# Kernel optimization log

Measured on AMD Instinct MI355X. Metric: run time of the kernel, lower is better.

## Reference

```python
import jax, jax.numpy as jnp
import numpy as np

B, T, C, H = 2, 2048, 1024, 16
D = C // H  # head dim = 64


def setup_inputs() -> dict:
    key = jax.random.key(0)
    ks = jax.random.split(key, 5)
    s = 0.02
    return {
        "x": jax.random.normal(ks[0], (B, T, C), dtype=jnp.float32),
        "c_attn_w": jax.random.normal(ks[1], (C, 3 * C), dtype=jnp.float32) * s,
        "c_attn_b": jax.random.normal(ks[2], (3 * C,), dtype=jnp.float32) * s,
        "c_proj_w": jax.random.normal(ks[3], (C, C), dtype=jnp.float32) * s,
        "c_proj_b": jax.random.normal(ks[4], (C,), dtype=jnp.float32) * s,
    }


def reference(x, c_attn_w, c_attn_b, c_proj_w, c_proj_b):
    b, t, c = x.shape
    # GPT-2 Conv1D: x @ W + b
    qkv = x @ c_attn_w + c_attn_b                      # [B,T,3C]
    q, k, v = jnp.split(qkv, 3, axis=-1)
    # [B,H,T,D]
    q = q.reshape(b, t, H, D).transpose(0, 2, 1, 3)
    k = k.reshape(b, t, H, D).transpose(0, 2, 1, 3)
    v = v.reshape(b, t, H, D).transpose(0, 2, 1, 3)
    scale = 1.0 / jnp.sqrt(jnp.float32(D))
    scores = jnp.einsum("bhqd,bhkd->bhqk", q, k) * scale  # [B,H,T,T]
    causal = jnp.tril(jnp.ones((t, t), dtype=bool))
    scores = jnp.where(causal, scores, jnp.float32(-jnp.inf))
    attn = jax.nn.softmax(scores, axis=-1)
    # drop_rate = 0.0 -> dropout is identity
    y = jnp.einsum("bhqk,bhkd->bhqd", attn, v)          # [B,H,T,D]
    y = y.transpose(0, 2, 1, 3).reshape(b, t, c)
    return y @ c_proj_w + c_proj_b
```

## Files before the change

kernel.cpp:

```cpp
#include <hip/hip_runtime.h>

#define B_ 2
#define T_ 2048
#define C_ 1024
#define H_ 16
#define D_ 64
#define M_ (B_ * T_)
#define NQKV_ (3 * C_)

typedef unsigned short us16;
typedef short bf16x8 __attribute__((ext_vector_type(8)));
typedef float f32x4 __attribute__((ext_vector_type(4)));

__device__ __forceinline__ f32x4 mfma16(bf16x8 a, bf16x8 b, f32x4 c) {
    return __builtin_amdgcn_mfma_f32_16x16x32_bf16(a, b, c, 0, 0, 0);
}

__device__ __forceinline__ us16 f2bf(float f) {
    union { float f; unsigned int u; } v; v.f = f;
    unsigned int r = v.u + 0x7fffu + ((v.u >> 16) & 1u);
    return (us16)(r >> 16);
}

__global__ __launch_bounds__(256) void cvt_bf16(
    const float* __restrict__ in, us16* __restrict__ out, int n8)
{
    const int i = blockIdx.x * blockDim.x + threadIdx.x;
    if (i >= n8) return;
    const float4 a = ((const float4*)in)[2 * i];
    const float4 b = ((const float4*)in)[2 * i + 1];
    ushort4 lo = { f2bf(a.x), f2bf(a.y), f2bf(a.z), f2bf(a.w) };
    ushort4 hi = { f2bf(b.x), f2bf(b.y), f2bf(b.z), f2bf(b.w) };
    ((ushort4*)out)[2 * i] = lo;
    ((ushort4*)out)[2 * i + 1] = hi;
}

__global__ __launch_bounds__(256) void transpose_cvt(
    const float* __restrict__ W, us16* __restrict__ Wt, int K, int N)
{
    __shared__ float tile[32][33];
    const int n0 = blockIdx.x * 32, k0 = blockIdx.y * 32;
    const int t = threadIdx.x;
    {
        const int k = t >> 3, n4 = (t & 7) * 4;
        const float4 v = *(const float4*)(W + (size_t)(k0 + k) * N + n0 + n4);
        tile[k][n4 + 0] = v.x; tile[k][n4 + 1] = v.y;
        tile[k][n4 + 2] = v.z; tile[k][n4 + 3] = v.w;
    }
    __syncthreads();
    {
        const int n = t >> 3, k4 = (t & 7) * 4;
        ushort4 o = { f2bf(tile[k4 + 0][n]), f2bf(tile[k4 + 1][n]),
                      f2bf(tile[k4 + 2][n]), f2bf(tile[k4 + 3][n]) };
        *(ushort4*)(Wt + (size_t)(n0 + n) * K + k0 + k4) = o;
    }
}

__global__ __launch_bounds__(256) void gemm_bf16(
    const us16* __restrict__ A, const us16* __restrict__ Bt,
    const float* __restrict__ bias, void* __restrict__ Cout,
    int M, int N, int K, int out_bf16)
{
    __shared__ __align__(16) us16 smem[2 * 128 * 72];
    us16* sA = smem;
    us16* sB = smem + 128 * 72;

    const int tid = threadIdx.x;
    const int lane = tid & 63, wave = tid >> 6;
    const int wr = wave >> 1, wc = wave & 1;
    const int cq = lane & 15, quad = lane >> 4;
    const int m0 = blockIdx.y * 128, n0 = blockIdx.x * 128;

    f32x4 acc[4][4];
    #pragma unroll
    for (int i = 0; i < 4; ++i)
        #pragma unroll
        for (int j = 0; j < 4; ++j)
            acc[i][j] = (f32x4){0.f, 0.f, 0.f, 0.f};

    for (int k0 = 0; k0 < K; k0 += 64) {
        #pragma unroll
        for (int p = 0; p < 4; ++p) {
            const int chunk = p * 256 + tid;
            const int r = chunk >> 3, c8 = (chunk & 7) * 8;
            const uint4 va = *(const uint4*)(A + (size_t)(m0 + r) * K + k0 + c8);
            *(uint4*)(sA + r * 72 + c8) = va;
            const uint4 vb = *(const uint4*)(Bt + (size_t)(n0 + r) * K + k0 + c8);
            *(uint4*)(sB + r * 72 + c8) = vb;
        }
        __syncthreads();

        #pragma unroll
        for (int kk = 0; kk < 64; kk += 32) {
            const int ko = kk + quad * 8;
            bf16x8 af[4], bfg[4];
            #pragma unroll
            for (int i = 0; i < 4; ++i) {
                af[i]  = *(const bf16x8*)(sA + (wr * 64 + i * 16 + cq) * 72 + ko);
                bfg[i] = *(const bf16x8*)(sB + (wc * 64 + i * 16 + cq) * 72 + ko);
            }
            #pragma unroll
            for (int mi = 0; mi < 4; ++mi)
                #pragma unroll
                for (int ni = 0; ni < 4; ++ni)
                    acc[mi][ni] = mfma16(af[mi], bfg[ni], acc[mi][ni]);
        }
        __syncthreads();
    }

    if (out_bf16) {
        us16* Cs = smem;
        #pragma unroll
        for (int mi = 0; mi < 4; ++mi)
            #pragma unroll
            for (int ni = 0; ni < 4; ++ni) {
                const int n = n0 + wc * 64 + ni * 16 + cq;
                const float bv = bias[n];
                #pragma unroll
                for (int r = 0; r < 4; ++r)
                    Cs[(wr * 64 + mi * 16 + quad * 4 + r) * 136 +
                       wc * 64 + ni * 16 + cq] = f2bf(acc[mi][ni][r] + bv);
            }
        __syncthreads();
        us16* Co = (us16*)Cout;
        #pragma unroll
        for (int p = 0; p < 8; ++p) {
            const int chunk = p * 256 + tid;
            const int r = chunk >> 4, c = (chunk & 15) * 8;
            *(uint4*)(Co + (size_t)(m0 + r) * N + n0 + c) =
                *(const uint4*)(Cs + r * 136 + c);
        }
    } else {
        float* Co = (float*)Cout;
        #pragma unroll
        for (int mi = 0; mi < 4; ++mi)
            #pragma unroll
            for (int ni = 0; ni < 4; ++ni) {
                const int n = n0 + wc * 64 + ni * 16 + cq;
                const float bv = bias[n];
                #pragma unroll
                for (int r = 0; r < 4; ++r)
                    Co[(size_t)(m0 + wr * 64 + mi * 16 + quad * 4 + r) * N + n] =
                        acc[mi][ni][r] + bv;
            }
    }
}

__global__ __launch_bounds__(256) void attn_mfma(
    const us16* __restrict__ qkv, us16* __restrict__ y)
{
    __shared__ __align__(16) us16 Ks[64][72];
    __shared__ __align__(16) us16 Vt[64][72];
    __shared__ __align__(16) us16 Ps[64][72];

    const int tid = threadIdx.x;
    const int lane = tid & 63, wave = tid >> 6;
    const int cq = lane & 15, quad = lane >> 4;
    const int bh = blockIdx.x;
    const int qt = (int)gridDim.y - 1 - (int)blockIdx.y;
    const int b = bh >> 4, h = bh & 15;

    const us16* base = qkv + (size_t)b * T_ * NQKV_ + h * D_;

    bf16x8 qf[2];
    {
        const us16* qrow = base + (size_t)(qt * 64 + wave * 16 + cq) * NQKV_;
        qf[0] = *(const bf16x8*)(qrow + quad * 8);
        qf[1] = *(const bf16x8*)(qrow + 32 + quad * 8);
    }

    f32x4 o[4];
    #pragma unroll
    for (int j = 0; j < 4; ++j) o[j] = (f32x4){0.f, 0.f, 0.f, 0.f};
    float m_run[4], l_run[4];
    #pragma unroll
    for (int r = 0; r < 4; ++r) { m_run[r] = -1e30f; l_run[r] = 0.f; }

    const int t2 = tid & 31, dc = tid >> 5;

    for (int kt = 0; kt <= qt; ++kt) {
        __syncthreads();
        #pragma unroll
        for (int p = 0; p < 2; ++p) {
            const int chunk = p * 256 + tid;
            const int r = chunk >> 3, c8 = (chunk & 7) * 8;
            const uint4 v = *(const uint4*)(base + (size_t)(kt * 64 + r) * NQKV_ + C_ + c8);
            *(uint4*)(&Ks[r][c8]) = v;
        }
        {
            const us16* vp = base + (size_t)(kt * 64 + 2 * t2) * NQKV_ + 2 * C_ + dc * 8;
            const uint4 u0 = *(const uint4*)vp;
            const uint4 u1 = *(const uint4*)(vp + NQKV_);
            const us16* p0 = (const us16*)&u0;
            const us16* p1 = (const us16*)&u1;
            #pragma unroll
            for (int j = 0; j < 8; ++j) {
                const unsigned int packed =
                    (unsigned int)p0[j] | ((unsigned int)p1[j] << 16);
                *(unsigned int*)(&Vt[dc * 8 + j][2 * t2]) = packed;
            }
        }
        __syncthreads();

        f32x4 s[4];
        #pragma unroll
        for (int j = 0; j < 4; ++j) {
            const bf16x8 kf0 = *(const bf16x8*)(&Ks[j * 16 + cq][quad * 8]);
            const bf16x8 kf1 = *(const bf16x8*)(&Ks[j * 16 + cq][32 + quad * 8]);
            f32x4 t = (f32x4){0.f, 0.f, 0.f, 0.f};
            t = mfma16(qf[0], kf0, t);
            t = mfma16(qf[1], kf1, t);
            s[j] = t;
        }

        #pragma unroll
        for (int j = 0; j < 4; ++j)
            #pragma unroll
            for (int r = 0; r < 4; ++r)
                s[j][r] *= 0.125f;
        if (kt == qt) {
            const int qloc = wave * 16 + quad * 4;
            #pragma unroll
            for (int j = 0; j < 4; ++j) {
                const int kloc = j * 16 + cq;
                #pragma unroll
                for (int r = 0; r < 4; ++r)
                    if (kloc > qloc + r) s[j][r] = -1e30f;
            }
        }

        #pragma unroll
        for (int r = 0; r < 4; ++r) {
            float mx = fmaxf(fmaxf(s[0][r], s[1][r]), fmaxf(s[2][r], s[3][r]));
            #pragma unroll
            for (int off = 8; off >= 1; off >>= 1)
                mx = fmaxf(mx, __shfl_xor(mx, off));
            const float m_new = fmaxf(m_run[r], mx);
            const float alpha = __expf(m_run[r] - m_new);
            float sum = 0.f;
            #pragma unroll
            for (int j = 0; j < 4; ++j) {
                s[j][r] = __expf(s[j][r] - m_new);
                sum += s[j][r];
            }
            #pragma unroll
            for (int off = 8; off >= 1; off >>= 1)
                sum += __shfl_xor(sum, off);
            l_run[r] = l_run[r] * alpha + sum;
            m_run[r] = m_new;
            #pragma unroll
            for (int j = 0; j < 4; ++j) o[j][r] *= alpha;
        }

        #pragma unroll
        for (int j = 0; j < 4; ++j)
            #pragma unroll
            for (int r = 0; r < 4; ++r)
                Ps[wave * 16 + quad * 4 + r][j * 16 + cq] = f2bf(s[j][r]);

        const bf16x8 pf0 = *(const bf16x8*)(&Ps[wave * 16 + cq][quad * 8]);
        const bf16x8 pf1 = *(const bf16x8*)(&Ps[wave * 16 + cq][32 + quad * 8]);
        #pragma unroll
        for (int dt = 0; dt < 4; ++dt) {
            const bf16x8 vf0 = *(const bf16x8*)(&Vt[dt * 16 + cq][quad * 8]);
            const bf16x8 vf1 = *(const bf16x8*)(&Vt[dt * 16 + cq][32 + quad * 8]);
            o[dt] = mfma16(pf0, vf0, o[dt]);
            o[dt] = mfma16(pf1, vf1, o[dt]);
        }
    }

    #pragma unroll
    for (int r = 0; r < 4; ++r) {
        const float inv = 1.0f / l_run[r];
        const int row = qt * 64 + wave * 16 + quad * 4 + r;
        #pragma unroll
        for (int dt = 0; dt < 4; ++dt)
            y[(size_t)(b * T_ + row) * C_ + h * D_ + dt * 16 + cq] =
                f2bf(o[dt][r] * inv);
    }
}

extern "C" void kernel_launch(void* const* d_in, const int* in_sizes, int n_in,
                              void* d_out, int out_size, void* d_ws, size_t ws_size,
                              hipStream_t stream)
{
    const float* x  = (const float*)d_in[0];
    const float* aw = (const float*)d_in[1];
    const float* ab = (const float*)d_in[2];
    const float* pw = (const float*)d_in[3];
    const float* pb = (const float*)d_in[4];
    float* out = (float*)d_out;

    us16* xb   = (us16*)d_ws;
    us16* awT  = xb  + (size_t)M_ * C_;
    us16* pwT  = awT + (size_t)NQKV_ * C_;
    us16* qkvb = pwT + (size_t)C_ * C_;
    us16* yb   = qkvb + (size_t)M_ * NQKV_;

    cvt_bf16<<<(M_ * C_ / 8 + 255) / 256, 256, 0, stream>>>(x, xb, M_ * C_ / 8);
    transpose_cvt<<<dim3(NQKV_ / 32, C_ / 32), 256, 0, stream>>>(aw, awT, C_, NQKV_);
    transpose_cvt<<<dim3(C_ / 32, C_ / 32), 256, 0, stream>>>(pw, pwT, C_, C_);

    gemm_bf16<<<dim3(NQKV_ / 128, M_ / 128), 256, 0, stream>>>(
        xb, awT, ab, qkvb, M_, NQKV_, C_, 1);

    attn_mfma<<<dim3(B_ * H_, T_ / 64), 256, 0, stream>>>(qkvb, yb);

    gemm_bf16<<<dim3(C_ / 128, M_ / 128), 256, 0, stream>>>(
        yb, pwT, pb, out, M_, C_, C_, 0);
}
```

Baseline: 222.8 us.

## Use direct-to-LDS swizzled loads in GEMM and pair query tiles in attention

The GEMM now uses global_load_lds to copy A/B tiles straight into an XOR-swizzled, unpadded LDS layout, which removes the register round trip and bank conflicts. The attention kernel pairs a short and a long causal query tile in each block so the work per block is balanced and each K/V tile load serves both. It also computes S transposed so the row max and sum need only two cross-lane shuffles, uses exp2 with the log2e factor folded into the scale, and packs P to bf16 by truncation instead of rounding. In exchange, P loses a little precision, the attention kernel holds more registers, and it runs half as many blocks.

After: 226.4 us. Within noise of the previous version (+1.6%).

```diff
diff --git a/kernel.cpp b/kernel.cpp
--- a/kernel.cpp
+++ b/kernel.cpp
@@ -9,6 +9,7 @@
 #define NQKV_ (3 * C_)
 
 typedef unsigned short us16;
+typedef unsigned int u32;
 typedef short bf16x8 __attribute__((ext_vector_type(8)));
 typedef float f32x4 __attribute__((ext_vector_type(4)));
 
@@ -17,9 +18,18 @@
 }
 
 __device__ __forceinline__ us16 f2bf(float f) {
-    union { float f; unsigned int u; } v; v.f = f;
-    unsigned int r = v.u + 0x7fffu + ((v.u >> 16) & 1u);
+    union { float f; u32 u; } v; v.f = f;
+    u32 r = v.u + 0x7fffu + ((v.u >> 16) & 1u);
     return (us16)(r >> 16);
+}
+__device__ __forceinline__ u32 fbits(float f) {
+    union { float f; u32 u; } v; v.f = f; return v.u;
+}
+
+typedef __attribute__((address_space(1))) const void as1_cvoid;
+typedef __attribute__((address_space(3))) void as3_void;
+__device__ __forceinline__ void gload_lds16(const us16* g, us16* l) {
+    __builtin_amdgcn_global_load_lds((as1_cvoid*)g, (as3_void*)l, 16, 0, 0);
 }
 
 __global__ __launch_bounds__(256) void cvt_bf16(
@@ -61,9 +71,9 @@
     const float* __restrict__ bias, void* __restrict__ Cout,
     int M, int N, int K, int out_bf16)
 {
-    __shared__ __align__(16) us16 smem[2 * 128 * 72];
+    __shared__ __align__(16) us16 smem[17408];
     us16* sA = smem;
-    us16* sB = smem + 128 * 72;
+    us16* sB = smem + 128 * 64;
 
     const int tid = threadIdx.x;
     const int lane = tid & 63, wave = tid >> 6;
@@ -71,6 +81,9 @@
     const int cq = lane & 15, quad = lane >> 4;
     const int m0 = blockIdx.y * 128, n0 = blockIdx.x * 128;
 
+    const int srow = lane >> 3;
+    const int schunk = (lane & 7) ^ srow;
+
     f32x4 acc[4][4];
     #pragma unroll
     for (int i = 0; i < 4; ++i)
@@ -80,24 +93,25 @@
 
     for (int k0 = 0; k0 < K; k0 += 64) {
         #pragma unroll
-        for (int p = 0; p < 4; ++p) {
-            const int chunk = p * 256 + tid;
-            const int r = chunk >> 3, c8 = (chunk & 7) * 8;
-            const uint4 va = *(const uint4*)(A + (size_t)(m0 + r) * K + k0 + c8);
-            *(uint4*)(sA + r * 72 + c8) = va;
-            const uint4 vb = *(const uint4*)(Bt + (size_t)(n0 + r) * K + k0 + c8);
-            *(uint4*)(sB + r * 72 + c8) = vb;
+        for (int i = 0; i < 4; ++i) {
+            const int r0 = wave * 32 + i * 8;
+            gload_lds16(A + (size_t)(m0 + r0 + srow) * K + k0 + schunk * 8,
+                        sA + r0 * 64);
+            gload_lds16(Bt + (size_t)(n0 + r0 + srow) * K + k0 + schunk * 8,
+                        sB + r0 * 64);
         }
         __syncthreads();
 
         #pragma unroll
         for (int kk = 0; kk < 64; kk += 32) {
-            const int ko = kk + quad * 8;
+            const int cb = kk >> 3;
             bf16x8 af[4], bfg[4];
             #pragma unroll
             for (int i = 0; i < 4; ++i) {
-                af[i]  = *(const bf16x8*)(sA + (wr * 64 + i * 16 + cq) * 72 + ko);
-                bfg[i] = *(const bf16x8*)(sB + (wc * 64 + i * 16 + cq) * 72 + ko);
+                const int ra = wr * 64 + i * 16 + cq;
+                af[i] = *(const bf16x8*)(sA + ra * 64 + (((cb + quad) ^ (cq & 7)) * 8));
+                const int rb = wc * 64 + i * 16 + cq;
+                bfg[i] = *(const bf16x8*)(sB + rb * 64 + (((cb + quad) ^ (cq & 7)) * 8));
             }
             #pragma unroll
             for (int mi = 0; mi < 4; ++mi)
@@ -146,6 +160,82 @@
     }
 }
 
+#define SCALE_LOG2E 0.1803368801111729f
+
+__device__ __forceinline__ void attn_step(
+    const us16 (*Ks)[72], const us16 (*Vt)[72], us16 (*Ps)[72],
+    const bf16x8* qf, float& m_run, float& l_run, f32x4* o,
+    int wave, int cq, int quad, bool diag)
+{
+    float s[4][4];
+    #pragma unroll
+    for (int j = 0; j < 4; ++j) {
+        const bf16x8 k0 = *(const bf16x8*)(&Ks[j * 16 + cq][quad * 8]);
+        const bf16x8 k1 = *(const bf16x8*)(&Ks[j * 16 + cq][32 + quad * 8]);
+        f32x4 t = (f32x4){0.f, 0.f, 0.f, 0.f};
+        t = mfma16(k0, qf[0], t);
+        t = mfma16(k1, qf[1], t);
+        #pragma unroll
+        for (int r = 0; r < 4; ++r) s[j][r] = t[r] * SCALE_LOG2E;
+    }
+
+    if (diag) {
+        const int q = wave * 16 + cq;
+        #pragma unroll
+        for (int j = 0; j < 4; ++j)
+            #pragma unroll
+            for (int r = 0; r < 4; ++r)
+                if (j * 16 + quad * 4 + r > q) s[j][r] = -1e30f;
+    }
+
+    float mx = s[0][0];
+    #pragma unroll
+    for (int j = 0; j < 4; ++j)
+        #pragma unroll
+        for (int r = 0; r < 4; ++r) mx = fmaxf(mx, s[j][r]);
+    mx = fmaxf(mx, __shfl_xor(mx, 16));
+    mx = fmaxf(mx, __shfl_xor(mx, 32));
+    const float m_new = fmaxf(m_run, mx);
+    const float alpha = exp2f(m_run - m_new);
+    float sum = 0.f;
+    #pragma unroll
+    for (int j = 0; j < 4; ++j)
+        #pragma unroll
+        for (int r = 0; r < 4; ++r) {
+            s[j][r] = exp2f(s[j][r] - m_new);
+            sum += s[j][r];
+        }
+    sum += __shfl_xor(sum, 16);
+    sum += __shfl_xor(sum, 32);
+    l_run = l_run * alpha + sum;
+    m_run = m_new;
+
+    #pragma unroll
+    for (int r = 0; r < 4; ++r) {
+        const float ar = __shfl(alpha, 20 * quad + r);
+        #pragma unroll
+        for (int dt = 0; dt < 4; ++dt) o[dt][r] *= ar;
+    }
+
+    #pragma unroll
+    for (int j = 0; j < 4; ++j) {
+        const u32 u0 = (fbits(s[j][1]) & 0xffff0000u) | (fbits(s[j][0]) >> 16);
+        const u32 u1 = (fbits(s[j][3]) & 0xffff0000u) | (fbits(s[j][2]) >> 16);
+        *(u32*)(&Ps[wave * 16 + cq][j * 16 + quad * 4]) = u0;
+        *(u32*)(&Ps[wave * 16 + cq][j * 16 + quad * 4 + 2]) = u1;
+    }
+
+    const bf16x8 p0 = *(const bf16x8*)(&Ps[wave * 16 + cq][quad * 8]);
+    const bf16x8 p1 = *(const bf16x8*)(&Ps[wave * 16 + cq][32 + quad * 8]);
+    #pragma unroll
+    for (int dt = 0; dt < 4; ++dt) {
+        const bf16x8 v0 = *(const bf16x8*)(&Vt[dt * 16 + cq][quad * 8]);
+        const bf16x8 v1 = *(const bf16x8*)(&Vt[dt * 16 + cq][32 + quad * 8]);
+        o[dt] = mfma16(p0, v0, o[dt]);
+        o[dt] = mfma16(p1, v1, o[dt]);
+    }
+}
+
 __global__ __launch_bounds__(256) void attn_mfma(
     const us16* __restrict__ qkv, us16* __restrict__ y)
 {
@@ -157,28 +247,33 @@
     const int lane = tid & 63, wave = tid >> 6;
     const int cq = lane & 15, quad = lane >> 4;
     const int bh = blockIdx.x;
-    const int qt = (int)gridDim.y - 1 - (int)blockIdx.y;
+    const int pr = blockIdx.y;
+    const int qtA = pr, qtB = (T_ / 64 - 1) - pr;
     const int b = bh >> 4, h = bh & 15;
 
     const us16* base = qkv + (size_t)b * T_ * NQKV_ + h * D_;
 
-    bf16x8 qf[2];
+    bf16x8 qA[2], qB[2];
     {
-        const us16* qrow = base + (size_t)(qt * 64 + wave * 16 + cq) * NQKV_;
-        qf[0] = *(const bf16x8*)(qrow + quad * 8);
-        qf[1] = *(const bf16x8*)(qrow + 32 + quad * 8);
-    }
-
-    f32x4 o[4];
-    #pragma unroll
-    for (int j = 0; j < 4; ++j) o[j] = (f32x4){0.f, 0.f, 0.f, 0.f};
-    float m_run[4], l_run[4];
-    #pragma unroll
-    for (int r = 0; r < 4; ++r) { m_run[r] = -1e30f; l_run[r] = 0.f; }
+        const us16* ra = base + (size_t)(qtA * 64 + wave * 16 + cq) * NQKV_;
+        qA[0] = *(const bf16x8*)(ra + quad * 8);
+        qA[1] = *(const bf16x8*)(ra + 32 + quad * 8);
+        const us16* rb = base + (size_t)(qtB * 64 + wave * 16 + cq) * NQKV_;
+        qB[0] = *(const bf16x8*)(rb + quad * 8);
+        qB[1] = *(const bf16x8*)(rb + 32 + quad * 8);
+    }
+
+    f32x4 oA[4], oB[4];
+    #pragma unroll
+    for (int j = 0; j < 4; ++j) {
+        oA[j] = (f32x4){0.f, 0.f, 0.f, 0.f};
+        oB[j] = (f32x4){0.f, 0.f, 0.f, 0.f};
+    }
+    float mA = -1e30f, lA = 0.f, mB = -1e30f, lB = 0.f;
 
     const int t2 = tid & 31, dc = tid >> 5;
 
-    for (int kt = 0; kt <= qt; ++kt) {
+    for (int kt = 0; kt <= qtB; ++kt) {
         __syncthreads();
         #pragma unroll
         for (int p = 0; p < 2; ++p) {
@@ -195,88 +290,29 @@
             const us16* p1 = (const us16*)&u1;
             #pragma unroll
             for (int j = 0; j < 8; ++j) {
-                const unsigned int packed =
-                    (unsigned int)p0[j] | ((unsigned int)p1[j] << 16);
-                *(unsigned int*)(&Vt[dc * 8 + j][2 * t2]) = packed;
+                const u32 packed = (u32)p0[j] | ((u32)p1[j] << 16);
+                *(u32*)(&Vt[dc * 8 + j][2 * t2]) = packed;
             }
         }
         __syncthreads();
 
-        f32x4 s[4];
-        #pragma unroll
-        for (int j = 0; j < 4; ++j) {
-            const bf16x8 kf0 = *(const bf16x8*)(&Ks[j * 16 + cq][quad * 8]);
-            const bf16x8 kf1 = *(const bf16x8*)(&Ks[j * 16 + cq][32 + quad * 8]);
-            f32x4 t = (f32x4){0.f, 0.f, 0.f, 0.f};
-            t = mfma16(qf[0], kf0, t);
-            t = mfma16(qf[1], kf1, t);
-            s[j] = t;
-        }
-
-        #pragma unroll
-        for (int j = 0; j < 4; ++j)
-            #pragma unroll
-            for (int r = 0; r < 4; ++r)
-                s[j][r] *= 0.125f;
-        if (kt == qt) {
-            const int qloc = wave * 16 + quad * 4;
-            #pragma unroll
-            for (int j = 0; j < 4; ++j) {
-                const int kloc = j * 16 + cq;
-                #pragma unroll
-                for (int r = 0; r < 4; ++r)
-                    if (kloc > qloc + r) s[j][r] = -1e30f;
-            }
-        }
-
-        #pragma unroll
-        for (int r = 0; r < 4; ++r) {
-            float mx = fmaxf(fmaxf(s[0][r], s[1][r]), fmaxf(s[2][r], s[3][r]));
-            #pragma unroll
-            for (int off = 8; off >= 1; off >>= 1)
-                mx = fmaxf(mx, __shfl_xor(mx, off));
-            const float m_new = fmaxf(m_run[r], mx);
-            const float alpha = __expf(m_run[r] - m_new);
-            float sum = 0.f;
-            #pragma unroll
-            for (int j = 0; j < 4; ++j) {
-                s[j][r] = __expf(s[j][r] - m_new);
-                sum += s[j][r];
-            }
-            #pragma unroll
-            for (int off = 8; off >= 1; off >>= 1)
-                sum += __shfl_xor(sum, off);
-            l_run[r] = l_run[r] * alpha + sum;
-            m_run[r] = m_new;
-            #pragma unroll
-            for (int j = 0; j < 4; ++j) o[j][r] *= alpha;
-        }
-
-        #pragma unroll
-        for (int j = 0; j < 4; ++j)
-            #pragma unroll
-            for (int r = 0; r < 4; ++r)
-                Ps[wave * 16 + quad * 4 + r][j * 16 + cq] = f2bf(s[j][r]);
-
-        const bf16x8 pf0 = *(const bf16x8*)(&Ps[wave * 16 + cq][quad * 8]);
-        const bf16x8 pf1 = *(const bf16x8*)(&Ps[wave * 16 + cq][32 + quad * 8]);
+        if (kt <= qtA)
+            attn_step(Ks, Vt, Ps, qA, mA, lA, oA, wave, cq, quad, kt == qtA);
+        attn_step(Ks, Vt, Ps, qB, mB, lB, oB, wave, cq, quad, kt == qtB);
+    }
+
+    const float invA = 1.0f / lA, invB = 1.0f / lB;
+    #pragma unroll
+    for (int r = 0; r < 4; ++r) {
+        const float iA = __shfl(invA, 20 * quad + r);
+        const float iB = __shfl(invB, 20 * quad + r);
+        const int rowA = qtA * 64 + wave * 16 + quad * 4 + r;
+        const int rowB = qtB * 64 + wave * 16 + quad * 4 + r;
         #pragma unroll
         for (int dt = 0; dt < 4; ++dt) {
-            const bf16x8 vf0 = *(const bf16x8*)(&Vt[dt * 16 + cq][quad * 8]);
-            const bf16x8 vf1 = *(const bf16x8*)(&Vt[dt * 16 + cq][32 + quad * 8]);
-            o[dt] = mfma16(pf0, vf0, o[dt]);
-            o[dt] = mfma16(pf1, vf1, o[dt]);
-        }
-    }
-
-    #pragma unroll
-    for (int r = 0; r < 4; ++r) {
-        const float inv = 1.0f / l_run[r];
-        const int row = qt * 64 + wave * 16 + quad * 4 + r;
-        #pragma unroll
-        for (int dt = 0; dt < 4; ++dt)
-            y[(size_t)(b * T_ + row) * C_ + h * D_ + dt * 16 + cq] =
-                f2bf(o[dt][r] * inv);
+            y[(size_t)(b * T_ + rowA) * C_ + h * D_ + dt * 16 + cq] = f2bf(oA[dt][r] * iA);
+            y[(size_t)(b * T_ + rowB) * C_ + h * D_ + dt * 16 + cq] = f2bf(oB[dt][r] * iB);
+        }
     }
 }
 
@@ -304,7 +340,7 @@
     gemm_bf16<<<dim3(NQKV_ / 128, M_ / 128), 256, 0, stream>>>(
         xb, awT, ab, qkvb, M_, NQKV_, C_, 1);
 
-    attn_mfma<<<dim3(B_ * H_, T_ / 64), 256, 0, stream>>>(qkvb, yb);
+    attn_mfma<<<dim3(B_ * H_, T_ / 128), 256, 0, stream>>>(qkvb, yb);
 
     gemm_bf16<<<dim3(C_ / 128, M_ / 128), 256, 0, stream>>>(
         yb, pwT, pb, out, M_, C_, C_, 0);
```
